# Optimization experiments

Hardware: AMD Instinct MI355X
Metric: run time of the kernel (lower is better)

## Reference

```python
import jax, jax.numpy as jnp
import numpy as np

EPS = 1e-5        # LayerNorm eps (torch default)
BETA = 1.0e12     # Hopfield scaling -> near-hard nearest-pattern retrieval


def _ln(x, g, b):
    mu = jnp.mean(x, axis=-1, keepdims=True)
    var = jnp.var(x, axis=-1, keepdims=True)
    return (x - mu) * jax.lax.rsqrt(var + EPS) * g + b


def setup_inputs() -> dict:
    key = jax.random.key(0)
    ks = jax.random.split(key, 10)
    B, S, D_IN, Q, P, D_OUT, N_CLS = 32768, 16, 14, 256, 256, 28, 7

    def n(k, shape, scale=1.0):
        return jax.random.normal(k, shape, dtype=jnp.float32) * scale

    return {
        "x": n(ks[0], (B, S, D_IN)),                 # (batch, bands=16, 14)
        "lookup": n(ks[1], (1, Q, D_IN)),            # learned stored patterns
        "g_st": jnp.ones((D_IN,), jnp.float32),      # LN stored pattern
        "b_st": jnp.zeros((D_IN,), jnp.float32),
        "g_sp": jnp.ones((D_IN,), jnp.float32),      # LN state pattern
        "b_sp": jnp.zeros((D_IN,), jnp.float32),
        "g_pp": jnp.ones((D_IN,), jnp.float32),      # LN pattern projection
        "b_pp": jnp.zeros((D_IN,), jnp.float32),
        "Wv": n(ks[2], (P, D_IN), 1.0 / np.sqrt(D_IN)),   # value proj 14->256 (no bias)
        "Wo": n(ks[3], (D_OUT, P), 1.0 / np.sqrt(P)),     # out proj 256->28 (no bias)
        "Wm": n(ks[4], (N_CLS, D_OUT), 1.0 / np.sqrt(D_OUT)),  # Linear_m 28->7
        "bm": n(ks[5], (N_CLS,), 0.1),
        "Wb": n(ks[6], (1, S), 1.0 / np.sqrt(S)),          # Linear_b 16->1
        "bb": n(ks[7], (1,), 0.1),
    }


def reference(x, lookup, g_st, b_st, g_sp, b_sp, g_pp, b_pp,
              Wv, Wo, Wm, bm, Wb, bb):
    # --- HopfieldLayer (num_heads=1, static Q/K, projected V) ---
    q = _ln(x, g_sp, b_sp)                       # state pattern, (B,S,14)
    k = _ln(lookup[0], g_st, b_st)               # stored patterns, (Q,14)
    v = _ln(lookup[0], g_pp, b_pp) @ Wv.T        # (Q,256)
    logits = BETA * jnp.einsum('bsd,qd->bsq', q, k)   # (B,S,Q)
    attn = jax.nn.softmax(logits, axis=-1)       # near one-hot retrieval
    h = jnp.einsum('bsq,qp->bsp', attn, v)       # (B,S,256)
    hop = h @ Wo.T                                # (B,S,28)
    # --- head ---
    y = hop @ Wm.T + bm                           # (B,S,7)
    y = jnp.swapaxes(y, 1, 2)                     # (B,7,S) == einsum 'abc->acb'
    z = y @ Wb.T + bb                             # (B,7,1)
    return jax.nn.softmax(z[:, :, 0], axis=1)     # (B,7)
```

## Files before the change

### kernel.cpp

```cpp
#include <hip/hip_runtime.h>
#include <math.h>

#define BATCH 32768
#define SS 16
#define DI 14
#define BQ 256
#define NC 7
#define NBLK 2048

#define WS_MPACK_OFF 0
#define WS_TF_OFF    28672
#define WS_ZB_OFF    35840
#define WS_CV_OFF    35896
#define WS_HC_OFF    37944

typedef float  f32x4 __attribute__((ext_vector_type(4)));
typedef short  s16x8 __attribute__((ext_vector_type(8)));
typedef float  v2f   __attribute__((ext_vector_type(2)));

__device__ __forceinline__ unsigned short bf16_rne(float f) {
    unsigned u = __float_as_uint(f);
    unsigned r = u + 0x7FFFu + ((u >> 16) & 1u);
    return (unsigned short)(r >> 16);
}
__device__ __forceinline__ float bf16_to_f32(unsigned short h) {
    return __uint_as_float(((unsigned)h) << 16);
}

__device__ __forceinline__ unsigned key32(float v, int j) {
    unsigned u = __float_as_uint(v);
    u ^= ((unsigned)((int)u >> 31)) | 0x80000000u;
    return (u & 0xFFFFFF00u) | (unsigned)(255 - j);
}

template<int PAT>
__device__ __forceinline__ unsigned swz(unsigned v) {
    return (unsigned)__builtin_amdgcn_ds_swizzle((int)v, PAT);
}

__global__ __launch_bounds__(256) void precompute_kernel(
    const float* __restrict__ lookup,
    const float* __restrict__ g_st, const float* __restrict__ b_st,
    const float* __restrict__ g_pp, const float* __restrict__ b_pp,
    const float* __restrict__ g_sp, const float* __restrict__ b_sp,
    const float* __restrict__ Wv,  const float* __restrict__ Wo,
    const float* __restrict__ Wm,  const float* __restrict__ bm,
    const float* __restrict__ Wb,  const float* __restrict__ bb,
    double2* __restrict__ mpack, float* __restrict__ Tf, double* __restrict__ zb,
    double* __restrict__ cvec, int* __restrict__ hc)
{
    __shared__ double G1s[256][7];
    __shared__ double Gs[14][7];
    const int tid = threadIdx.x;

    {
        const int p = tid;
        for (int c = 0; c < NC; ++c) {
            double acc = 0.0;
            for (int o = 0; o < 28; ++o)
                acc += (double)Wo[o * 256 + p] * (double)Wm[c * 28 + o];
            G1s[p][c] = acc;
        }
    }
    __syncthreads();
    if (tid < DI * NC) {
        const int d = tid / NC, c = tid % NC;
        double acc = 0.0;
        for (int p = 0; p < 256; ++p)
            acc += (double)Wv[p * DI + d] * G1s[p][c];
        Gs[d][c] = acc;
    }
    __syncthreads();

    {
        const int j = tid;
        double xr[DI];
        double sum = 0.0;
        for (int d = 0; d < DI; ++d) { xr[d] = (double)lookup[j * DI + d]; sum += xr[d]; }
        const double mu = sum * (1.0 / (double)DI);
        double vs = 0.0;
        for (int d = 0; d < DI; ++d) { const double t = xr[d] - mu; vs += t * t; }
        const double rs = 1.0 / sqrt(vs * (1.0 / (double)DI) + 1e-5);

        double kj[DI], vl[DI];
        for (int d = 0; d < DI; ++d) {
            const double nrm = (xr[d] - mu) * rs;
            kj[d] = nrm * (double)g_st[d] + (double)b_st[d];
            vl[d] = nrm * (double)g_pp[d] + (double)b_pp[d];
        }
        double mv[DI], S = 0.0, cj = 0.0;
        for (int d = 0; d < DI; ++d) {
            mv[d] = kj[d] * (double)g_sp[d];
            S += mv[d];
            cj += (double)b_sp[d] * kj[d];
        }
        const double Sm = S * (1.0 / (double)DI);
        for (int d2 = 0; d2 < DI / 2; ++d2) {
            double2 p; p.x = mv[2 * d2] - Sm; p.y = mv[2 * d2 + 1] - Sm;
            mpack[d2 * 256 + j] = p;
        }
        cvec[j] = cj;

        for (int c = 0; c < NC; ++c) {
            double acc = 0.0;
            for (int d = 0; d < DI; ++d) acc += vl[d] * Gs[d][c];
            Tf[j * NC + c] = (float)acc;
        }
    }
    if (tid < NC) {
        double wbsum = 0.0;
        for (int s = 0; s < SS; ++s) wbsum += (double)Wb[s];
        zb[tid] = (double)bm[tid] * wbsum + (double)bb[0];
    }
    if (tid == 0) {
        int f = 0;
        for (int d = 0; d < DI; ++d) f |= (b_sp[d] != 0.0f) ? 1 : 0;
        *hc = f;
    }
}

__global__ __launch_bounds__(256, 4) void hopfield_kernel(
    const float* __restrict__ x,
    const double2* __restrict__ mpack, const double* __restrict__ cvec,
    const int* __restrict__ hcp,
    const float* __restrict__ Tf, const double* __restrict__ zb,
    const float* __restrict__ Wb, float* __restrict__ out)
{
    __shared__ s16x8  bhiS[16 * 32];
    __shared__ s16x8  bloS[16 * 32];
    __shared__ double zbs[NC];
    __shared__ float  wbs[SS];
    __shared__ int    jcandS[4][4][SS][2];
    __shared__ int    jstarS[4][4][SS];
    __shared__ double zrowd[4][4][NC];
    __shared__ float  irsS[4][4][SS];

    const int tid  = threadIdx.x;
    const int lane = tid & 63;
    const int w    = tid >> 6;
    const int g    = lane >> 4;
    const int l    = lane & 15;
    const int hc   = *hcp;

    {
        const int j = tid;
        float mf[16];
        #pragma unroll
        for (int d2 = 0; d2 < 7; ++d2) {
            const double2 mv = mpack[d2 * 256 + j];
            mf[2 * d2] = (float)mv.x; mf[2 * d2 + 1] = (float)mv.y;
        }
        mf[14] = (float)cvec[j];
        mf[15] = 0.f;
        #pragma unroll
        for (int ks = 0; ks < 2; ++ks) {
            s16x8 h8, l8;
            #pragma unroll
            for (int i = 0; i < 8; ++i) {
                const float f = mf[8 * ks + i];
                const unsigned short h = bf16_rne(f);
                const float r = f - bf16_to_f32(h);
                h8[i] = (short)h;
                l8[i] = (short)bf16_rne(r);
            }
            bhiS[(j >> 4) * 32 + ks * 16 + (j & 15)] = h8;
            bloS[(j >> 4) * 32 + ks * 16 + (j & 15)] = l8;
        }
    }
    if (tid < NC) zbs[tid] = zb[tid];
    if (tid < SS) wbs[tid] = Wb[tid];
    __syncthreads();

    const int gw = blockIdx.x * 4 + w;
    const float* xw = x + (size_t)gw * 4 * SS * DI;

    if (hc) {
        const int bi = lane >> 4, s = lane & 15;
        const float* xr = xw + (bi * SS + s) * DI;
        float xv[DI]; float sum = 0.f;
        #pragma unroll
        for (int d = 0; d < DI; ++d) { xv[d] = xr[d]; sum += xv[d]; }
        const float mu = sum * (1.0f / (float)DI);
        float vs = 0.f;
        #pragma unroll
        for (int d = 0; d < DI; ++d) { const float t = xv[d] - mu; vs += t * t; }
        irsS[w][bi][s] = 1.0f / sqrtf(vs * (1.0f / (float)DI) + 1e-5f);
        __builtin_amdgcn_wave_barrier();
    }

    for (int bi = 0; bi < 4; ++bi) {
        s16x8 xh = {0,0,0,0,0,0,0,0}, xl = {0,0,0,0,0,0,0,0};
        if (lane < 32) {
            const float* xr = xw + (bi * SS + l) * DI;
            float xv[8];
            if (g == 0) {
                #pragma unroll
                for (int i = 0; i < 4; ++i) {
                    const v2f p = *(const v2f*)(xr + 2 * i);
                    xv[2 * i] = p.x; xv[2 * i + 1] = p.y;
                }
            } else {
                #pragma unroll
                for (int i = 0; i < 3; ++i) {
                    const v2f p = *(const v2f*)(xr + 8 + 2 * i);
                    xv[2 * i] = p.x; xv[2 * i + 1] = p.y;
                }
                xv[6] = hc ? irsS[w][bi][l] : 0.f;
                xv[7] = 0.f;
            }
            #pragma unroll
            for (int i = 0; i < 8; ++i) {
                const unsigned short h = bf16_rne(xv[i]);
                const float r = xv[i] - bf16_to_f32(h);
                xh[i] = (short)h;
                xl[i] = (short)bf16_rne(r);
            }
        }

        float tv[4][2]; int ti[4][2];
        #pragma unroll
        for (int r = 0; r < 4; ++r) {
            tv[r][0] = -INFINITY; tv[r][1] = -INFINITY;
            ti[r][0] = 0;         ti[r][1] = 1;
        }
        const f32x4 z4 = {0.f, 0.f, 0.f, 0.f};

        #pragma unroll
        for (int t = 0; t < 16; ++t) {
            s16x8 ph = {0,0,0,0,0,0,0,0}, pl = {0,0,0,0,0,0,0,0};
            if (lane < 32) { ph = bhiS[t * 32 + lane]; pl = bloS[t * 32 + lane]; }
            f32x4 acc = __builtin_amdgcn_mfma_f32_16x16x32_bf16(pl, xh, z4, 0, 0, 0);
            acc = __builtin_amdgcn_mfma_f32_16x16x32_bf16(ph, xl, acc, 0, 0, 0);
            acc = __builtin_amdgcn_mfma_f32_16x16x32_bf16(ph, xh, acc, 0, 0, 0);
            #pragma unroll
            for (int r = 0; r < 4; ++r) {
                const float s = acc[r];
                if (t & 1) {
                    const bool c = s > tv[r][1];
                    tv[r][1] = c ? s : tv[r][1]; ti[r][1] = c ? t : ti[r][1];
                } else {
                    const bool c = s > tv[r][0];
                    tv[r][0] = c ? s : tv[r][0]; ti[r][0] = c ? t : ti[r][0];
                }
            }
        }

        const int jbase = (lane & 0x30) >> 2;
        unsigned h4[4], l4[4];
        #pragma unroll
        for (int r = 0; r < 4; ++r) {
            const unsigned k0 = key32(tv[r][0], ti[r][0] * 16 + jbase + r);
            const unsigned k1 = key32(tv[r][1], ti[r][1] * 16 + jbase + r);
            h4[r] = k0 > k1 ? k0 : k1;
            l4[r] = k0 > k1 ? k1 : k0;
        }
        unsigned H0, L0, H1, L1, kh, kl;
        {   const unsigned mn = h4[0] < h4[1] ? h4[0] : h4[1];
            H0 = h4[0] > h4[1] ? h4[0] : h4[1];
            const unsigned mx = l4[0] > l4[1] ? l4[0] : l4[1];
            L0 = mn > mx ? mn : mx; }
        {   const unsigned mn = h4[2] < h4[3] ? h4[2] : h4[3];
            H1 = h4[2] > h4[3] ? h4[2] : h4[3];
            const unsigned mx = l4[2] > l4[3] ? l4[2] : l4[3];
            L1 = mn > mx ? mn : mx; }
        {   const unsigned mn = H0 < H1 ? H0 : H1;
            kh = H0 > H1 ? H0 : H1;
            const unsigned mx = L0 > L1 ? L0 : L1;
            kl = mn > mx ? mn : mx; }

        {
            const unsigned oh = swz<0x401F>(kh), ol = swz<0x401F>(kl);
            const unsigned mn = kh < oh ? kh : oh;
            kh = kh > oh ? kh : oh;
            const unsigned mx = kl > ol ? kl : ol;
            kl = mn > mx ? mn : mx;
        }
        {
            const unsigned oh = (unsigned)__shfl_xor((int)kh, 32);
            const unsigned ol = (unsigned)__shfl_xor((int)kl, 32);
            const unsigned mn = kh < oh ? kh : oh;
            kh = kh > oh ? kh : oh;
            const unsigned mx = kl > ol ? kl : ol;
            kl = mn > mx ? mn : mx;
        }
        if (lane < 16) {
            jcandS[w][bi][lane][0] = 255 - (int)(kh & 0xFFu);
            jcandS[w][bi][lane][1] = 255 - (int)(kl & 0xFFu);
        }
    }
    __builtin_amdgcn_wave_barrier();

    #pragma unroll
    for (int u = 0; u < 2; ++u) {
        const int task = u * 64 + lane;
        const int bi = task >> 5, row = (task >> 1) & 15, ci = task & 1;
        const int j = jcandS[w][bi][row][ci];
        const float* xr = xw + (bi * SS + row) * DI;
        double a = 0.0;
        #pragma unroll
        for (int d2 = 0; d2 < 7; ++d2) {
            const v2f xp = *(const v2f*)(xr + 2 * d2);
            const double2 mv = mpack[d2 * 256 + j];
            a += (double)xp.x * mv.x + (double)xp.y * mv.y;
        }
        if (hc) {
            double xv[DI]; double sum = 0.0;
            #pragma unroll
            for (int d = 0; d < DI; ++d) { xv[d] = (double)xr[d]; sum += xv[d]; }
            const double mu = sum * (1.0 / (double)DI);
            double vs = 0.0;
            #pragma unroll
            for (int d = 0; d < DI; ++d) { const double t = xv[d] - mu; vs += t * t; }
            const double irs64 = 1.0 / sqrt(vs * (1.0 / (double)DI) + 1e-5);
            a += irs64 * cvec[j];
        }
        const double oa = __shfl_xor(a, 1);
        const int    oj = __shfl_xor(j, 1);
        const int jwin = (a > oa || (a == oa && j < oj)) ? j : oj;
        if ((lane & 1) == 0) jstarS[w][bi][row] = jwin;
    }
    __builtin_amdgcn_wave_barrier();

    if (lane < 4 * NC) {
        const int bi = lane / NC, c = lane % NC;
        double zv = zbs[c];
        #pragma unroll
        for (int s = 0; s < SS; ++s)
            zv += (double)wbs[s] * (double)Tf[jstarS[w][bi][s] * NC + c];
        zrowd[w][bi][c] = zv;
    }
    __builtin_amdgcn_wave_barrier();
    if (lane < 4 * NC) {
        const int bi = lane / NC;
        double m = zrowd[w][bi][0];
        #pragma unroll
        for (int c2 = 1; c2 < NC; ++c2) m = fmax(m, zrowd[w][bi][c2]);
        float den = 0.f;
        #pragma unroll
        for (int c2 = 0; c2 < NC; ++c2) den += __expf((float)(zrowd[w][bi][c2] - m));
        const float num = __expf((float)(zrowd[w][bi][lane % NC] - m));
        out[(size_t)gw * 28 + lane] = num / den;
    }
}

extern "C" void kernel_launch(void* const* d_in, const int* in_sizes, int n_in,
                              void* d_out, int out_size, void* d_ws, size_t ws_size,
                              hipStream_t stream) {
    const float* x      = (const float*)d_in[0];
    const float* lookup = (const float*)d_in[1];
    const float* g_st   = (const float*)d_in[2];
    const float* b_st   = (const float*)d_in[3];
    const float* g_sp   = (const float*)d_in[4];
    const float* b_sp   = (const float*)d_in[5];
    const float* g_pp   = (const float*)d_in[6];
    const float* b_pp   = (const float*)d_in[7];
    const float* Wv     = (const float*)d_in[8];
    const float* Wo     = (const float*)d_in[9];
    const float* Wm     = (const float*)d_in[10];
    const float* bm     = (const float*)d_in[11];
    const float* Wb     = (const float*)d_in[12];
    const float* bb     = (const float*)d_in[13];

    double2* mpack = (double2*)((char*)d_ws + WS_MPACK_OFF);
    float*   Tf    = (float*)((char*)d_ws + WS_TF_OFF);
    double*  zbp   = (double*)((char*)d_ws + WS_ZB_OFF);
    double*  cvec  = (double*)((char*)d_ws + WS_CV_OFF);
    int*     hc    = (int*)((char*)d_ws + WS_HC_OFF);

    precompute_kernel<<<1, 256, 0, stream>>>(lookup, g_st, b_st, g_pp, b_pp,
                                             g_sp, b_sp,
                                             Wv, Wo, Wm, bm, Wb, bb,
                                             mpack, Tf, zbp, cvec, hc);
    hopfield_kernel<<<NBLK, 256, 0, stream>>>(x, mpack, cvec, hc, Tf, zbp, Wb,
                                              (float*)d_out);
}
```

Measured before the change: 150.4 us.

## Switch pattern scoring to 32x32x16 MFMA processing two batch rows per pass

Replaces the 16x16x32 bf16 MFMA scoring, which left half the lanes idle and looped over four batch rows, with 32x32x16 MFMAs that cover two batch rows (32 columns) per pass using all 64 lanes. The stored-pattern LDS layout is reorganized into 32-pattern tiles, and the top-2 candidate reduction now runs mostly in registers across 16 accumulator rows, dropping the ds_swizzle step. The intent is better MFMA lane utilization and fewer instructions per batch row. In exchange it uses more registers for accumulators and top-2 tracking, which may reduce occupancy.

Result: slower. 166.9 us (+10.9%).

```diff
diff --git a/kernel.cpp b/kernel.cpp
--- a/kernel.cpp
+++ b/kernel.cpp
@@ -14,9 +14,9 @@
 #define WS_CV_OFF    35896
 #define WS_HC_OFF    37944
 
-typedef float  f32x4 __attribute__((ext_vector_type(4)));
-typedef short  s16x8 __attribute__((ext_vector_type(8)));
-typedef float  v2f   __attribute__((ext_vector_type(2)));
+typedef float  f32x16 __attribute__((ext_vector_type(16)));
+typedef short  s16x8  __attribute__((ext_vector_type(8)));
+typedef float  v2f    __attribute__((ext_vector_type(2)));
 
 __device__ __forceinline__ unsigned short bf16_rne(float f) {
     unsigned u = __float_as_uint(f);
@@ -31,11 +31,6 @@
     unsigned u = __float_as_uint(v);
     u ^= ((unsigned)((int)u >> 31)) | 0x80000000u;
     return (u & 0xFFFFFF00u) | (unsigned)(255 - j);
-}
-
-template<int PAT>
-__device__ __forceinline__ unsigned swz(unsigned v) {
-    return (unsigned)__builtin_amdgcn_ds_swizzle((int)v, PAT);
 }
 
 __global__ __launch_bounds__(256) void precompute_kernel(
@@ -126,8 +121,8 @@
     const float* __restrict__ Tf, const double* __restrict__ zb,
     const float* __restrict__ Wb, float* __restrict__ out)
 {
-    __shared__ s16x8  bhiS[16 * 32];
-    __shared__ s16x8  bloS[16 * 32];
+    __shared__ s16x8  bhiS[8 * 64];
+    __shared__ s16x8  bloS[8 * 64];
     __shared__ double zbs[NC];
     __shared__ float  wbs[SS];
     __shared__ int    jcandS[4][4][SS][2];
@@ -138,8 +133,6 @@
     const int tid  = threadIdx.x;
     const int lane = tid & 63;
     const int w    = tid >> 6;
-    const int g    = lane >> 4;
-    const int l    = lane & 15;
     const int hc   = *hcp;
 
     {
@@ -163,8 +156,8 @@
                 h8[i] = (short)h;
                 l8[i] = (short)bf16_rne(r);
             }
-            bhiS[(j >> 4) * 32 + ks * 16 + (j & 15)] = h8;
-            bloS[(j >> 4) * 32 + ks * 16 + (j & 15)] = l8;
+            bhiS[(j >> 5) * 64 + ks * 32 + (j & 31)] = h8;
+            bloS[(j >> 5) * 64 + ks * 32 + (j & 31)] = l8;
         }
     }
     if (tid < NC) zbs[tid] = zb[tid];
@@ -188,12 +181,19 @@
         __builtin_amdgcn_wave_barrier();
     }
 
-    for (int bi = 0; bi < 4; ++bi) {
-        s16x8 xh = {0,0,0,0,0,0,0,0}, xl = {0,0,0,0,0,0,0,0};
-        if (lane < 32) {
-            const float* xr = xw + (bi * SS + l) * DI;
+    const int col = lane & 31;
+    const int khf = lane >> 5;
+    const int jadd = khf << 2;
+
+    for (int pr = 0; pr < 2; ++pr) {
+        const int bi   = pr * 2 + (col >> 4);
+        const int band = col & 15;
+
+        s16x8 xbh, xbl;
+        {
+            const float* xr = xw + (bi * SS + band) * DI;
             float xv[8];
-            if (g == 0) {
+            if (khf == 0) {
                 #pragma unroll
                 for (int i = 0; i < 4; ++i) {
                     const v2f p = *(const v2f*)(xr + 2 * i);
@@ -205,76 +205,68 @@
                     const v2f p = *(const v2f*)(xr + 8 + 2 * i);
                     xv[2 * i] = p.x; xv[2 * i + 1] = p.y;
                 }
-                xv[6] = hc ? irsS[w][bi][l] : 0.f;
+                xv[6] = hc ? irsS[w][bi][band] : 0.f;
                 xv[7] = 0.f;
             }
             #pragma unroll
             for (int i = 0; i < 8; ++i) {
                 const unsigned short h = bf16_rne(xv[i]);
                 const float r = xv[i] - bf16_to_f32(h);
-                xh[i] = (short)h;
-                xl[i] = (short)bf16_rne(r);
-            }
-        }
-
-        float tv[4][2]; int ti[4][2];
-        #pragma unroll
-        for (int r = 0; r < 4; ++r) {
-            tv[r][0] = -INFINITY; tv[r][1] = -INFINITY;
-            ti[r][0] = 0;         ti[r][1] = 1;
-        }
-        const f32x4 z4 = {0.f, 0.f, 0.f, 0.f};
-
-        #pragma unroll
-        for (int t = 0; t < 16; ++t) {
-            s16x8 ph = {0,0,0,0,0,0,0,0}, pl = {0,0,0,0,0,0,0,0};
-            if (lane < 32) { ph = bhiS[t * 32 + lane]; pl = bloS[t * 32 + lane]; }
-            f32x4 acc = __builtin_amdgcn_mfma_f32_16x16x32_bf16(pl, xh, z4, 0, 0, 0);
-            acc = __builtin_amdgcn_mfma_f32_16x16x32_bf16(ph, xl, acc, 0, 0, 0);
-            acc = __builtin_amdgcn_mfma_f32_16x16x32_bf16(ph, xh, acc, 0, 0, 0);
-            #pragma unroll
-            for (int r = 0; r < 4; ++r) {
+                xbh[i] = (short)h;
+                xbl[i] = (short)bf16_rne(r);
+            }
+        }
+
+        float tv[16]; int ti[16];
+        #pragma unroll
+        for (int r = 0; r < 16; ++r) { tv[r] = -INFINITY; ti[r] = 0; }
+
+        f32x16 z16;
+        #pragma unroll
+        for (int r = 0; r < 16; ++r) z16[r] = 0.f;
+
+        #pragma unroll
+        for (int t = 0; t < 8; ++t) {
+            const s16x8 ph = bhiS[t * 64 + lane];
+            const s16x8 pl = bloS[t * 64 + lane];
+            f32x16 acc = __builtin_amdgcn_mfma_f32_32x32x16_bf16(pl, xbh, z16, 0, 0, 0);
+            acc = __builtin_amdgcn_mfma_f32_32x32x16_bf16(ph, xbl, acc, 0, 0, 0);
+            acc = __builtin_amdgcn_mfma_f32_32x32x16_bf16(ph, xbh, acc, 0, 0, 0);
+            #pragma unroll
+            for (int r = 0; r < 16; ++r) {
                 const float s = acc[r];
-                if (t & 1) {
-                    const bool c = s > tv[r][1];
-                    tv[r][1] = c ? s : tv[r][1]; ti[r][1] = c ? t : ti[r][1];
-                } else {
-                    const bool c = s > tv[r][0];
-                    tv[r][0] = c ? s : tv[r][0]; ti[r][0] = c ? t : ti[r][0];
+                const bool c = s > tv[r];
+                tv[r] = c ? s : tv[r];
+                ti[r] = c ? t : ti[r];
+            }
+        }
+
+        unsigned hk[8], lk[8];
+        #pragma unroll
+        for (int r2 = 0; r2 < 8; ++r2) {
+            const int ra = 2 * r2, rb = 2 * r2 + 1;
+            const int ja = ti[ra] * 32 + ((ra & 3) + 8 * (ra >> 2)) + jadd;
+            const int jb = ti[rb] * 32 + ((rb & 3) + 8 * (rb >> 2)) + jadd;
+            const unsigned ka = key32(tv[ra], ja);
+            const unsigned kb = key32(tv[rb], jb);
+            hk[r2] = ka > kb ? ka : kb;
+            lk[r2] = ka > kb ? kb : ka;
+        }
+        #pragma unroll
+        for (int st = 4; st > 0; st >>= 1) {
+            #pragma unroll
+            for (int m = 0; m < 4; ++m) {
+                if (m < st) {
+                    const unsigned h1 = hk[m], h2 = hk[m + st];
+                    const unsigned l1 = lk[m], l2 = lk[m + st];
+                    const unsigned mn = h1 < h2 ? h1 : h2;
+                    hk[m] = h1 > h2 ? h1 : h2;
+                    const unsigned mx = l1 > l2 ? l1 : l2;
+                    lk[m] = mn > mx ? mn : mx;
                 }
             }
         }
-
-        const int jbase = (lane & 0x30) >> 2;
-        unsigned h4[4], l4[4];
-        #pragma unroll
-        for (int r = 0; r < 4; ++r) {
-            const unsigned k0 = key32(tv[r][0], ti[r][0] * 16 + jbase + r);
-            const unsigned k1 = key32(tv[r][1], ti[r][1] * 16 + jbase + r);
-            h4[r] = k0 > k1 ? k0 : k1;
-            l4[r] = k0 > k1 ? k1 : k0;
-        }
-        unsigned H0, L0, H1, L1, kh, kl;
-        {   const unsigned mn = h4[0] < h4[1] ? h4[0] : h4[1];
-            H0 = h4[0] > h4[1] ? h4[0] : h4[1];
-            const unsigned mx = l4[0] > l4[1] ? l4[0] : l4[1];
-            L0 = mn > mx ? mn : mx; }
-        {   const unsigned mn = h4[2] < h4[3] ? h4[2] : h4[3];
-            H1 = h4[2] > h4[3] ? h4[2] : h4[3];
-            const unsigned mx = l4[2] > l4[3] ? l4[2] : l4[3];
-            L1 = mn > mx ? mn : mx; }
-        {   const unsigned mn = H0 < H1 ? H0 : H1;
-            kh = H0 > H1 ? H0 : H1;
-            const unsigned mx = L0 > L1 ? L0 : L1;
-            kl = mn > mx ? mn : mx; }
-
-        {
-            const unsigned oh = swz<0x401F>(kh), ol = swz<0x401F>(kl);
-            const unsigned mn = kh < oh ? kh : oh;
-            kh = kh > oh ? kh : oh;
-            const unsigned mx = kl > ol ? kl : ol;
-            kl = mn > mx ? mn : mx;
-        }
+        unsigned kh = hk[0], kl = lk[0];
         {
             const unsigned oh = (unsigned)__shfl_xor((int)kh, 32);
             const unsigned ol = (unsigned)__shfl_xor((int)kl, 32);
@@ -283,9 +275,9 @@
             const unsigned mx = kl > ol ? kl : ol;
             kl = mn > mx ? mn : mx;
         }
-        if (lane < 16) {
-            jcandS[w][bi][lane][0] = 255 - (int)(kh & 0xFFu);
-            jcandS[w][bi][lane][1] = 255 - (int)(kl & 0xFFu);
+        if (lane < 32) {
+            jcandS[w][bi][band][0] = 255 - (int)(kh & 0xFFu);
+            jcandS[w][bi][band][1] = 255 - (int)(kl & 0xFFu);
         }
     }
     __builtin_amdgcn_wave_barrier();
```
